# Optimization experiments

Hardware: AMD Instinct MI355X
Metric: run time of the kernel (lower is better)

## Reference

```python
import jax, jax.numpy as jnp
import numpy as np

B, C, H, W = 8, 512, 64, 64
DEPTH, HEADS = 4, 8


def setup_inputs() -> dict:
    key = jax.random.key(0)
    ks = jax.random.split(key, 7)
    s = 0.02
    return {
        "x": jax.random.normal(ks[0], (B, C, H, W), jnp.float32),
        # axial positional embeddings, emb dim at index 1: (1,C,H,1) and (1,C,1,W)
        "pos_h": jax.random.normal(ks[1], (C, H), jnp.float32) * s,
        "pos_w": jax.random.normal(ks[2], (C, W), jnp.float32) * s,
        # per layer, per axis (0=height, 1=width): q, kv, out projections
        "wq": jax.random.normal(ks[3], (DEPTH, 2, C, C), jnp.float32) * s,
        "wkv": jax.random.normal(ks[4], (DEPTH, 2, C, 2 * C), jnp.float32) * s,
        "wo": jax.random.normal(ks[5], (DEPTH, 2, C, C), jnp.float32) * s,
        "wo_b": jax.random.normal(ks[6], (DEPTH, 2, C), jnp.float32) * s,
    }


def _attn_last_axis(x, wq, wkv, wo, wo_b, heads):
    """Self-attention along the second-to-last axis. x: (..., L, C)."""
    lead = x.shape[:-2]
    L, Cd = x.shape[-2], x.shape[-1]
    e = Cd // heads
    q = x @ wq                       # (..., L, C)
    k, v = jnp.split(x @ wkv, 2, axis=-1)
    sh = lead + (L, heads, e)
    q, k, v = q.reshape(sh), k.reshape(sh), v.reshape(sh)
    dots = jnp.einsum('...ihe,...jhe->...hij', q, k) * (e ** -0.5)
    attn = jax.nn.softmax(dots, axis=-1)
    out = jnp.einsum('...hij,...jhe->...ihe', attn, v).reshape(lead + (L, heads * e))
    return out @ wo + wo_b


def reference(x, pos_h, pos_w, wq, wkv, wo, wo_b):
    # positional embedding: x + (1,C,H,1) + (1,C,1,W)
    x = x + pos_h[None, :, :, None] + pos_w[None, :, None, :]
    y = jnp.transpose(x, (0, 2, 3, 1))  # (B,H,W,C) channels-last working layout
    for l in range(DEPTH):
        # height-axis attention: (B,W,H,C), attend along H
        yh = jnp.transpose(y, (0, 2, 1, 3))
        oh = _attn_last_axis(yh, wq[l, 0], wkv[l, 0], wo[l, 0], wo_b[l, 0], HEADS)
        oh = jnp.transpose(oh, (0, 2, 1, 3))
        # width-axis attention: attend along W
        ow = _attn_last_axis(y, wq[l, 1], wkv[l, 1], wo[l, 1], wo_b[l, 1], HEADS)
        y = oh + ow  # sum_axial_out=True, no residual
    return jnp.transpose(y, (0, 3, 1, 2))  # back to (B,C,H,W)
```

## Files before the change

kernel.cpp:

```cpp
#include <hip/hip_runtime.h>
#include <stdint.h>


typedef __attribute__((ext_vector_type(8))) short bf16x8;
typedef __attribute__((ext_vector_type(4))) float f32x4;
typedef unsigned short u16;
typedef unsigned int u32;

#define MFMA16(a, b, c) __builtin_amdgcn_mfma_f32_16x16x32_bf16((a), (b), (c), 0, 0, 0)
#define SBAR() __builtin_amdgcn_sched_barrier(0)

__device__ __forceinline__ float b2f(u16 h) {
    u32 u = ((u32)h) << 16;
    float f;
    __builtin_memcpy(&f, &u, 4);
    return f;
}
__device__ __forceinline__ u16 f2b(float f) {
    u32 u;
    __builtin_memcpy(&u, &f, 4);
    u32 r = (u + 0x7fffu + ((u >> 16) & 1u)) >> 16;
    return (u16)r;
}
__device__ __forceinline__ uint2 pack4(const f32x4& v) {
    uint2 pk;
    pk.x = (u32)f2b(v[0]) | ((u32)f2b(v[1]) << 16);
    pk.y = (u32)f2b(v[2]) | ((u32)f2b(v[3]) << 16);
    return pk;
}

#define GLD_LDS16(g, l)                                                        \
    __builtin_amdgcn_global_load_lds(                                          \
        (const __attribute__((address_space(1))) void*)(g),                    \
        (__attribute__((address_space(3))) void*)(l), 16, 0, 0)

__global__ __launch_bounds__(256) void embed_kernel(
    const float* __restrict__ x, const float* __restrict__ ph,
    const float* __restrict__ pw, u16* __restrict__ y)
{
    __shared__ float tile[64][65];
    const int c0 = blockIdx.x * 64, h = blockIdx.y, b = blockIdx.z;
    const int t = threadIdx.x;
#pragma unroll
    for (int i = 0; i < 4; ++i) {
        int cl = (t >> 4) + i * 16;
        int w4 = (t & 15) * 4;
        const float* src = x + (((size_t)(b * 512 + c0 + cl)) * 64 + h) * 64 + w4;
        float4 v = *(const float4*)src;
        float p = ph[(c0 + cl) * 64 + h];
        tile[cl][w4 + 0] = v.x + p + pw[(c0 + cl) * 64 + w4 + 0];
        tile[cl][w4 + 1] = v.y + p + pw[(c0 + cl) * 64 + w4 + 1];
        tile[cl][w4 + 2] = v.z + p + pw[(c0 + cl) * 64 + w4 + 2];
        tile[cl][w4 + 3] = v.w + p + pw[(c0 + cl) * 64 + w4 + 3];
    }
    __syncthreads();
    const int wl = t >> 2, cb = (t & 3) * 16;
    bf16x8 o0, o1;
#pragma unroll
    for (int j = 0; j < 8; ++j) o0[j] = (short)f2b(tile[cb + j][wl]);
#pragma unroll
    for (int j = 0; j < 8; ++j) o1[j] = (short)f2b(tile[cb + 8 + j][wl]);
    u16* dst = y + (((size_t)(b * 64 + h) * 64 + wl) * 512 + c0 + cb);
    *(bf16x8*)dst = o0;
    *(bf16x8*)(dst + 8) = o1;
}

__global__ __launch_bounds__(256) void wtrans_kernel(
    const float* __restrict__ wq, const float* __restrict__ wkv,
    const float* __restrict__ wo, u16* __restrict__ wT)
{
    const int mid = blockIdx.z;
    const int l = mid / 6, rest = mid % 6, axis = rest / 3, which = rest % 3;
    const size_t la = (size_t)(l * 2 + axis);
    const float* src;
    int N;
    size_t doff;
    if (which == 0)      { src = wq  + la * 512 * 512;  N = 512;  doff = la * (2048 * 512); }
    else if (which == 1) { src = wkv + la * 512 * 1024; N = 1024; doff = la * (2048 * 512) + 512 * 512; }
    else                 { src = wo  + la * 512 * 512;  N = 512;  doff = la * (2048 * 512) + 512 * 512 + 1024 * 512; }
    const int n0 = blockIdx.y * 64;
    if (n0 >= N) return;
    const int k0 = blockIdx.x * 64;
    __shared__ float tile[64][65];
    const int t = threadIdx.x;
#pragma unroll
    for (int i = 0; i < 4; ++i) {
        int kl = (t >> 4) + i * 16;
        int n4 = (t & 15) * 4;
        float4 v = *(const float4*)(src + (size_t)(k0 + kl) * N + n0 + n4);
        tile[kl][n4 + 0] = v.x; tile[kl][n4 + 1] = v.y;
        tile[kl][n4 + 2] = v.z; tile[kl][n4 + 3] = v.w;
    }
    __syncthreads();
    const int nl = t >> 2, kb = (t & 3) * 16;
    bf16x8 o0, o1;
#pragma unroll
    for (int j = 0; j < 8; ++j) o0[j] = (short)f2b(tile[kb + j][nl]);
#pragma unroll
    for (int j = 0; j < 8; ++j) o1[j] = (short)f2b(tile[kb + 8 + j][nl]);
    u16* dst = wT + doff + (size_t)(n0 + nl) * 512 + k0 + kb;
    *(bf16x8*)dst = o0;
    *(bf16x8*)(dst + 8) = o1;
}

template <int AXIS>
__global__ __launch_bounds__(512, 2) void fused_layer(
    const u16* __restrict__ y,
    const u16* __restrict__ wTla,
    const float* __restrict__ bias,
    u16* __restrict__ yout)
{
    __shared__ u16 LDS[65536];
    const int tid = threadIdx.x, lane = tid & 63, wid = tid >> 6;
    const int l16 = lane & 15, g = lane >> 4;
    const int bid = blockIdx.x;
    const size_t rowbase = ((size_t)(bid >> 6) << 12) +
                           (AXIS == 0 ? (size_t)(bid & 63) : ((size_t)(bid & 63) << 6));
    const int rowstr = (AXIS == 0) ? 64 : 1;

    u16* Ys = LDS;
    u16* scr = LDS + 32768 + wid * 4096;

#pragma unroll
    for (int i = 0; i < 8; ++i) {
        int row = wid * 8 + i;
        const u16* src = y + (rowbase + (size_t)row * rowstr) * 512 + ((lane ^ (row & 7)) << 3);
        GLD_LDS16(src, Ys + row * 512);
    }
    __syncthreads();

    const int hoff = wid * 64;
    const u16* wq_ = wTla + (size_t)hoff * 512;
    const u16* wk_ = wTla + (size_t)(512 + hoff) * 512;
    const u16* wv_ = wTla + (size_t)(512 + 512 + hoff) * 512;
    const u16* wo_ = wTla + (size_t)(512 + 1024) * 512;

#define YF(r, t) (*(const bf16x8*)((const char*)Ys + (r) * 1024 + \
                    ((((t) * 4 + g) ^ ((r) & 7)) << 4)))
#define SF(r, k2) (*(const bf16x8*)((const char*)scr + (r) * 128 + \
                    (((k2) * 64 + g * 16) ^ (((r) & 7) << 4))))

    f32x4 ak[4][4] = {}, aq[4][4] = {};
#pragma unroll
    for (int t = 0; t < 16; ++t) {
        bf16x8 yf[4], wkf[4], wqf[4];
#pragma unroll
        for (int f = 0; f < 4; ++f) {
            int row = f * 16 + l16;
            yf[f]  = YF(row, t);
            wkf[f] = *(const bf16x8*)(wk_ + (size_t)row * 512 + t * 32 + g * 8);
            wqf[f] = *(const bf16x8*)(wq_ + (size_t)row * 512 + t * 32 + g * 8);
        }
#pragma unroll
        for (int ef = 0; ef < 4; ++ef)
#pragma unroll
            for (int jf = 0; jf < 4; ++jf) {
                ak[ef][jf] = MFMA16(wkf[ef], yf[jf], ak[ef][jf]);
                aq[ef][jf] = MFMA16(wqf[ef], yf[jf], aq[ef][jf]);
            }
    }

#pragma unroll
    for (int ef = 0; ef < 4; ++ef)
#pragma unroll
        for (int jf = 0; jf < 4; ++jf) {
            int j = jf * 16 + l16, bo = (ef * 16 + g * 4) * 2;
            *(uint2*)((char*)scr + j * 128 + (bo ^ ((j & 7) << 4))) = pack4(ak[ef][jf]);
        }
    SBAR();
    bf16x8 kf[4][2];
#pragma unroll
    for (int jf = 0; jf < 4; ++jf)
#pragma unroll
        for (int k2 = 0; k2 < 2; ++k2) kf[jf][k2] = SF(jf * 16 + l16, k2);
    SBAR();
#pragma unroll
    for (int ef = 0; ef < 4; ++ef)
#pragma unroll
        for (int jf = 0; jf < 4; ++jf) {
            int j = jf * 16 + l16, bo = (ef * 16 + g * 4) * 2;
            *(uint2*)((char*)scr + j * 128 + (bo ^ ((j & 7) << 4))) = pack4(aq[ef][jf]);
        }
    SBAR();
    bf16x8 qf[4][2];
#pragma unroll
    for (int if_ = 0; if_ < 4; ++if_)
#pragma unroll
        for (int k2 = 0; k2 < 2; ++k2) qf[if_][k2] = SF(if_ * 16 + l16, k2);
    SBAR();

    f32x4 st[4][4] = {};
#pragma unroll
    for (int k2 = 0; k2 < 2; ++k2)
#pragma unroll
        for (int i_f = 0; i_f < 4; ++i_f)
#pragma unroll
            for (int j_f = 0; j_f < 4; ++j_f)
                st[i_f][j_f] = MFMA16(kf[j_f][k2], qf[i_f][k2], st[i_f][j_f]);

#pragma unroll
    for (int i_f = 0; i_f < 4; ++i_f) {
        const int irow = i_f * 16 + l16;
        float ev[4][4];
        float mx = -1e30f;
#pragma unroll
        for (int j_f = 0; j_f < 4; ++j_f)
#pragma unroll
            for (int r = 0; r < 4; ++r) {
                float v = st[i_f][j_f][r] * 0.125f;
                ev[j_f][r] = v;
                mx = fmaxf(mx, v);
            }
        mx = fmaxf(mx, __shfl_xor(mx, 16, 64));
        mx = fmaxf(mx, __shfl_xor(mx, 32, 64));
        float sum = 0.f;
#pragma unroll
        for (int j_f = 0; j_f < 4; ++j_f)
#pragma unroll
            for (int r = 0; r < 4; ++r) {
                float e = __expf(ev[j_f][r] - mx);
                ev[j_f][r] = e;
                sum += e;
            }
        sum += __shfl_xor(sum, 16, 64);
        sum += __shfl_xor(sum, 32, 64);
        float inv = __builtin_amdgcn_rcpf(sum);
#pragma unroll
        for (int j_f = 0; j_f < 4; ++j_f) {
            uint2 pk;
            pk.x = (u32)f2b(ev[j_f][0] * inv) | ((u32)f2b(ev[j_f][1] * inv) << 16);
            pk.y = (u32)f2b(ev[j_f][2] * inv) | ((u32)f2b(ev[j_f][3] * inv) << 16);
            int addr = irow * 128 + ((j_f * 32 + g * 8) ^ ((irow & 7) << 4));
            *(uint2*)((char*)scr + addr) = pk;
        }
    }
    SBAR();
    bf16x8 pf[4][2];
#pragma unroll
    for (int if_ = 0; if_ < 4; ++if_)
#pragma unroll
        for (int k2 = 0; k2 < 2; ++k2) pf[if_][k2] = SF(if_ * 16 + l16, k2);
    SBAR();

    f32x4 av[4][4] = {};
#pragma unroll
    for (int t = 0; t < 16; ++t) {
        bf16x8 yf[4], wvf[4];
#pragma unroll
        for (int f = 0; f < 4; ++f) {
            int row = f * 16 + l16;
            yf[f]  = YF(row, t);
            wvf[f] = *(const bf16x8*)(wv_ + (size_t)row * 512 + t * 32 + g * 8);
        }
#pragma unroll
        for (int jf = 0; jf < 4; ++jf)
#pragma unroll
            for (int ef = 0; ef < 4; ++ef)
                av[jf][ef] = MFMA16(yf[jf], wvf[ef], av[jf][ef]);
    }
#pragma unroll
    for (int jf = 0; jf < 4; ++jf)
#pragma unroll
        for (int ef = 0; ef < 4; ++ef) {
            int e = ef * 16 + l16, bo = (jf * 16 + g * 4) * 2;
            *(uint2*)((char*)scr + e * 128 + (bo ^ ((e & 7) << 4))) = pack4(av[jf][ef]);
        }
    SBAR();
    bf16x8 vtf[4][2];
#pragma unroll
    for (int ef = 0; ef < 4; ++ef)
#pragma unroll
        for (int k2 = 0; k2 < 2; ++k2) vtf[ef][k2] = SF(ef * 16 + l16, k2);
    SBAR();

    f32x4 of[4][4] = {};
#pragma unroll
    for (int k2 = 0; k2 < 2; ++k2)
#pragma unroll
        for (int ef = 0; ef < 4; ++ef)
#pragma unroll
            for (int i_f = 0; i_f < 4; ++i_f)
                of[ef][i_f] = MFMA16(vtf[ef][k2], pf[i_f][k2], of[ef][i_f]);

    __syncthreads();
#pragma unroll
    for (int ef = 0; ef < 4; ++ef)
#pragma unroll
        for (int i_f = 0; i_f < 4; ++i_f) {
            int i = i_f * 16 + l16;
            int bo = (hoff + ef * 16 + g * 4) * 2;
            *(uint2*)((char*)Ys + i * 1024 + (bo ^ ((i & 7) << 4))) = pack4(of[ef][i_f]);
        }
    __syncthreads();

    const int n0 = hoff;
    f32x4 ao[4][4] = {};
#pragma unroll
    for (int t = 0; t < 16; ++t) {
        bf16x8 off[4], wof[4];
#pragma unroll
        for (int f = 0; f < 4; ++f) {
            int row = f * 16 + l16;
            off[f] = YF(row, t);
            wof[f] = *(const bf16x8*)(wo_ + (size_t)(n0 + row) * 512 + t * 32 + g * 8);
        }
#pragma unroll
        for (int nf = 0; nf < 4; ++nf)
#pragma unroll
            for (int if_ = 0; if_ < 4; ++if_)
                ao[nf][if_] = MFMA16(wof[nf], off[if_], ao[nf][if_]);
    }

    float4 b4[4];
#pragma unroll
    for (int nf = 0; nf < 4; ++nf) b4[nf] = *(const float4*)(bias + n0 + nf * 16 + g * 4);
#pragma unroll
    for (int if_ = 0; if_ < 4; ++if_) {
        const int i = if_ * 16 + l16;
        u16* dst = yout + (rowbase + (size_t)i * rowstr) * 512;
#pragma unroll
        for (int nf = 0; nf < 4; ++nf) {
            const int n = n0 + nf * 16 + g * 4;
            float v0 = ao[nf][if_][0] + b4[nf].x;
            float v1 = ao[nf][if_][1] + b4[nf].y;
            float v2 = ao[nf][if_][2] + b4[nf].z;
            float v3 = ao[nf][if_][3] + b4[nf].w;
            if (AXIS == 1) {
                ushort4 o = *(const ushort4*)(dst + n);
                v0 += b2f(o.x); v1 += b2f(o.y); v2 += b2f(o.z); v3 += b2f(o.w);
            }
            uint2 pk;
            pk.x = (u32)f2b(v0) | ((u32)f2b(v1) << 16);
            pk.y = (u32)f2b(v2) | ((u32)f2b(v3) << 16);
            *(uint2*)(dst + n) = pk;
        }
    }
#undef YF
#undef SF
}

__global__ __launch_bounds__(256) void untrans_kernel(
    const u16* __restrict__ y, float* __restrict__ out)
{
    __shared__ float tile[64][65];
    const int c0 = blockIdx.x * 64, h = blockIdx.y, b = blockIdx.z;
    const int t = threadIdx.x;
    {
        const int wl = t >> 2, cb = (t & 3) * 16;
        const u16* src = y + (((size_t)(b * 64 + h) * 64 + wl) * 512 + c0 + cb);
        bf16x8 v0 = *(const bf16x8*)src;
        bf16x8 v1 = *(const bf16x8*)(src + 8);
#pragma unroll
        for (int j = 0; j < 8; ++j) tile[wl][cb + j] = b2f((u16)v0[j]);
#pragma unroll
        for (int j = 0; j < 8; ++j) tile[wl][cb + 8 + j] = b2f((u16)v1[j]);
    }
    __syncthreads();
    const int cl = t >> 2, w16 = (t & 3) * 16;
    float* dst = out + (((size_t)(b * 512 + c0 + cl)) * 64 + h) * 64 + w16;
#pragma unroll
    for (int j = 0; j < 4; ++j) {
        float4 v;
        v.x = tile[w16 + j * 4 + 0][cl];
        v.y = tile[w16 + j * 4 + 1][cl];
        v.z = tile[w16 + j * 4 + 2][cl];
        v.w = tile[w16 + j * 4 + 3][cl];
        *(float4*)(dst + j * 4) = v;
    }
}

extern "C" void kernel_launch(void* const* d_in, const int* in_sizes, int n_in,
                              void* d_out, int out_size, void* d_ws, size_t ws_size,
                              hipStream_t stream)
{
    (void)in_sizes; (void)n_in; (void)out_size; (void)ws_size;
    const float* x   = (const float*)d_in[0];
    const float* ph  = (const float*)d_in[1];
    const float* pw  = (const float*)d_in[2];
    const float* wq  = (const float*)d_in[3];
    const float* wkv = (const float*)d_in[4];
    const float* wo  = (const float*)d_in[5];
    const float* wob = (const float*)d_in[6];

    char* ws = (char*)d_ws;
    u16* yA = (u16*)(ws);
    u16* yB = (u16*)(ws + 33554432);
    u16* wT = (u16*)(ws + 67108864);
    float* out = (float*)d_out;

    embed_kernel<<<dim3(8, 64, 8), 256, 0, stream>>>(x, ph, pw, yA);
    wtrans_kernel<<<dim3(8, 16, 24), 256, 0, stream>>>(wq, wkv, wo, wT);

    u16* yin = yA;
    u16* yout = yB;
    for (int l = 0; l < 4; ++l) {
        for (int axis = 0; axis < 2; ++axis) {
            const u16* wTla = wT + (size_t)(l * 2 + axis) * 2048 * 512;
            const float* bias = wob + (size_t)(l * 2 + axis) * 512;
            if (axis == 0)
                fused_layer<0><<<dim3(512), 512, 0, stream>>>(yin, wTla, bias, yout);
            else
                fused_layer<1><<<dim3(512), 512, 0, stream>>>(yin, wTla, bias, yout);
        }
        u16* tmp = yin; yin = yout; yout = tmp;
    }
    untrans_kernel<<<dim3(8, 64, 8), 256, 0, stream>>>(yin, out);
}
```

Before: 1.222 ms.

## Split K and Q projections and shrink per-wave scratch to cut LDS and registers

The fused axial-attention layer kernel now computes the K and Q projections in two separate passes that share one accumulator array, instead of one pass holding both. This halves live accumulator registers. Each wave's LDS scratch shrinks from 64 rows to 16 rows, and the transposes through scratch are done one 16-row fragment at a time. Total LDS per block drops from 128KB to 80KB. The goal is lower register and LDS pressure so more blocks or waves can be resident, at the cost of reading the Y tile from LDS twice for K and Q and having more small write/read rounds through scratch.

```diff
diff --git a/kernel.cpp b/kernel.cpp
--- a/kernel.cpp
+++ b/kernel.cpp
@@ -110,7 +110,7 @@
     const float* __restrict__ bias,
     u16* __restrict__ yout)
 {
-    __shared__ u16 LDS[65536];
+    __shared__ u16 LDS[40960];
     const int tid = threadIdx.x, lane = tid & 63, wid = tid >> 6;
     const int l16 = lane & 15, g = lane >> 4;
     const int bid = blockIdx.x;
@@ -119,7 +119,7 @@
     const int rowstr = (AXIS == 0) ? 64 : 1;
 
     u16* Ys = LDS;
-    u16* scr = LDS + 32768 + wid * 4096;
+    u16* scr = LDS + 32768 + wid * 1024;
 
 #pragma unroll
     for (int i = 0; i < 8; ++i) {
@@ -137,57 +137,72 @@
 
 #define YF(r, t) (*(const bf16x8*)((const char*)Ys + (r) * 1024 + \
                     ((((t) * 4 + g) ^ ((r) & 7)) << 4)))
-#define SF(r, k2) (*(const bf16x8*)((const char*)scr + (r) * 128 + \
-                    (((k2) * 64 + g * 16) ^ (((r) & 7) << 4))))
-
-    f32x4 ak[4][4] = {}, aq[4][4] = {};
+#define SW16(bo, val) *(uint2*)((char*)scr + l16 * 128 + ((bo) ^ ((l16 & 7) << 4))) = (val)
+#define SF16(k2) (*(const bf16x8*)((const char*)scr + l16 * 128 + \
+                    (((k2) * 64 + g * 16) ^ ((l16 & 7) << 4))))
+
+    f32x4 acc[4][4];
+    bf16x8 kf[4][2], qf[4][2];
+
+#pragma unroll
+    for (int ef = 0; ef < 4; ++ef)
+#pragma unroll
+        for (int jf = 0; jf < 4; ++jf) acc[ef][jf] = f32x4{0.f, 0.f, 0.f, 0.f};
 #pragma unroll
     for (int t = 0; t < 16; ++t) {
-        bf16x8 yf[4], wkf[4], wqf[4];
+        bf16x8 yf[4], wf[4];
 #pragma unroll
         for (int f = 0; f < 4; ++f) {
             int row = f * 16 + l16;
-            yf[f]  = YF(row, t);
-            wkf[f] = *(const bf16x8*)(wk_ + (size_t)row * 512 + t * 32 + g * 8);
-            wqf[f] = *(const bf16x8*)(wq_ + (size_t)row * 512 + t * 32 + g * 8);
+            yf[f] = YF(row, t);
+            wf[f] = *(const bf16x8*)(wk_ + (size_t)row * 512 + t * 32 + g * 8);
         }
 #pragma unroll
         for (int ef = 0; ef < 4; ++ef)
 #pragma unroll
-            for (int jf = 0; jf < 4; ++jf) {
-                ak[ef][jf] = MFMA16(wkf[ef], yf[jf], ak[ef][jf]);
-                aq[ef][jf] = MFMA16(wqf[ef], yf[jf], aq[ef][jf]);
-            }
+            for (int jf = 0; jf < 4; ++jf)
+                acc[ef][jf] = MFMA16(wf[ef], yf[jf], acc[ef][jf]);
+    }
+#pragma unroll
+    for (int jf = 0; jf < 4; ++jf) {
+#pragma unroll
+        for (int ef = 0; ef < 4; ++ef)
+            SW16((ef * 16 + g * 4) * 2, pack4(acc[ef][jf]));
+        SBAR();
+        kf[jf][0] = SF16(0);
+        kf[jf][1] = SF16(1);
+        SBAR();
     }
 
 #pragma unroll
     for (int ef = 0; ef < 4; ++ef)
 #pragma unroll
-        for (int jf = 0; jf < 4; ++jf) {
-            int j = jf * 16 + l16, bo = (ef * 16 + g * 4) * 2;
-            *(uint2*)((char*)scr + j * 128 + (bo ^ ((j & 7) << 4))) = pack4(ak[ef][jf]);
-        }
-    SBAR();
-    bf16x8 kf[4][2];
-#pragma unroll
-    for (int jf = 0; jf < 4; ++jf)
-#pragma unroll
-        for (int k2 = 0; k2 < 2; ++k2) kf[jf][k2] = SF(jf * 16 + l16, k2);
-    SBAR();
-#pragma unroll
-    for (int ef = 0; ef < 4; ++ef)
-#pragma unroll
-        for (int jf = 0; jf < 4; ++jf) {
-            int j = jf * 16 + l16, bo = (ef * 16 + g * 4) * 2;
-            *(uint2*)((char*)scr + j * 128 + (bo ^ ((j & 7) << 4))) = pack4(aq[ef][jf]);
-        }
-    SBAR();
-    bf16x8 qf[4][2];
-#pragma unroll
-    for (int if_ = 0; if_ < 4; ++if_)
-#pragma unroll
-        for (int k2 = 0; k2 < 2; ++k2) qf[if_][k2] = SF(if_ * 16 + l16, k2);
-    SBAR();
+        for (int jf = 0; jf < 4; ++jf) acc[ef][jf] = f32x4{0.f, 0.f, 0.f, 0.f};
+#pragma unroll
+    for (int t = 0; t < 16; ++t) {
+        bf16x8 yf[4], wf[4];
+#pragma unroll
+        for (int f = 0; f < 4; ++f) {
+            int row = f * 16 + l16;
+            yf[f] = YF(row, t);
+            wf[f] = *(const bf16x8*)(wq_ + (size_t)row * 512 + t * 32 + g * 8);
+        }
+#pragma unroll
+        for (int ef = 0; ef < 4; ++ef)
+#pragma unroll
+            for (int jf = 0; jf < 4; ++jf)
+                acc[ef][jf] = MFMA16(wf[ef], yf[jf], acc[ef][jf]);
+    }
+#pragma unroll
+    for (int jf = 0; jf < 4; ++jf) {
+#pragma unroll
+        for (int ef = 0; ef < 4; ++ef)
+            SW16((ef * 16 + g * 4) * 2, pack4(acc[ef][jf]));
+        SBAR();
+        qf[jf][0] = SF16(0);
+        qf[jf][1] = SF16(1);
+        SBAR();
+    }
 
     f32x4 st[4][4] = {};
 #pragma unroll
@@ -198,9 +213,9 @@
             for (int j_f = 0; j_f < 4; ++j_f)
                 st[i_f][j_f] = MFMA16(kf[j_f][k2], qf[i_f][k2], st[i_f][j_f]);
 
+    bf16x8 pf[4][2];
 #pragma unroll
     for (int i_f = 0; i_f < 4; ++i_f) {
-        const int irow = i_f * 16 + l16;
         float ev[4][4];
         float mx = -1e30f;
 #pragma unroll
@@ -230,48 +245,44 @@
             uint2 pk;
             pk.x = (u32)f2b(ev[j_f][0] * inv) | ((u32)f2b(ev[j_f][1] * inv) << 16);
             pk.y = (u32)f2b(ev[j_f][2] * inv) | ((u32)f2b(ev[j_f][3] * inv) << 16);
-            int addr = irow * 128 + ((j_f * 32 + g * 8) ^ ((irow & 7) << 4));
-            *(uint2*)((char*)scr + addr) = pk;
-        }
-    }
-    SBAR();
-    bf16x8 pf[4][2];
-#pragma unroll
-    for (int if_ = 0; if_ < 4; ++if_)
-#pragma unroll
-        for (int k2 = 0; k2 < 2; ++k2) pf[if_][k2] = SF(if_ * 16 + l16, k2);
-    SBAR();
-
-    f32x4 av[4][4] = {};
+            SW16(j_f * 32 + g * 8, pk);
+        }
+        SBAR();
+        pf[i_f][0] = SF16(0);
+        pf[i_f][1] = SF16(1);
+        SBAR();
+    }
+
+#pragma unroll
+    for (int jf = 0; jf < 4; ++jf)
+#pragma unroll
+        for (int ef = 0; ef < 4; ++ef) acc[jf][ef] = f32x4{0.f, 0.f, 0.f, 0.f};
 #pragma unroll
     for (int t = 0; t < 16; ++t) {
-        bf16x8 yf[4], wvf[4];
+        bf16x8 yf[4], wf[4];
 #pragma unroll
         for (int f = 0; f < 4; ++f) {
             int row = f * 16 + l16;
-            yf[f]  = YF(row, t);
-            wvf[f] = *(const bf16x8*)(wv_ + (size_t)row * 512 + t * 32 + g * 8);
+            yf[f] = YF(row, t);
+            wf[f] = *(const bf16x8*)(wv_ + (size_t)row * 512 + t * 32 + g * 8);
         }
 #pragma unroll
         for (int jf = 0; jf < 4; ++jf)
 #pragma unroll
             for (int ef = 0; ef < 4; ++ef)
-                av[jf][ef] = MFMA16(yf[jf], wvf[ef], av[jf][ef]);
-    }
-#pragma unroll
-    for (int jf = 0; jf < 4; ++jf)
-#pragma unroll
-        for (int ef = 0; ef < 4; ++ef) {
-            int e = ef * 16 + l16, bo = (jf * 16 + g * 4) * 2;
-            *(uint2*)((char*)scr + e * 128 + (bo ^ ((e & 7) << 4))) = pack4(av[jf][ef]);
-        }
-    SBAR();
+                acc[jf][ef] = MFMA16(yf[jf], wf[ef], acc[jf][ef]);
+    }
     bf16x8 vtf[4][2];
 #pragma unroll
-    for (int ef = 0; ef < 4; ++ef)
-#pragma unroll
-        for (int k2 = 0; k2 < 2; ++k2) vtf[ef][k2] = SF(ef * 16 + l16, k2);
-    SBAR();
+    for (int ef = 0; ef < 4; ++ef) {
+#pragma unroll
+        for (int jf = 0; jf < 4; ++jf)
+            SW16((jf * 16 + g * 4) * 2, pack4(acc[jf][ef]));
+        SBAR();
+        vtf[ef][0] = SF16(0);
+        vtf[ef][1] = SF16(1);
+        SBAR();
+    }
 
     f32x4 of[4][4] = {};
 #pragma unroll
@@ -293,38 +304,40 @@
         }
     __syncthreads();
 
-    const int n0 = hoff;
-    f32x4 ao[4][4] = {};
+#pragma unroll
+    for (int nf = 0; nf < 4; ++nf)
+#pragma unroll
+        for (int if_ = 0; if_ < 4; ++if_) acc[nf][if_] = f32x4{0.f, 0.f, 0.f, 0.f};
 #pragma unroll
     for (int t = 0; t < 16; ++t) {
-        bf16x8 off[4], wof[4];
+        bf16x8 off[4], wf[4];
 #pragma unroll
         for (int f = 0; f < 4; ++f) {
             int row = f * 16 + l16;
             off[f] = YF(row, t);
-            wof[f] = *(const bf16x8*)(wo_ + (size_t)(n0 + row) * 512 + t * 32 + g * 8);
+            wf[f] = *(const bf16x8*)(wo_ + (size_t)(hoff + row) * 512 + t * 32 + g * 8);
         }
 #pragma unroll
         for (int nf = 0; nf < 4; ++nf)
 #pragma unroll
             for (int if_ = 0; if_ < 4; ++if_)
-                ao[nf][if_] = MFMA16(wof[nf], off[if_], ao[nf][if_]);
+                acc[nf][if_] = MFMA16(wf[nf], off[if_], acc[nf][if_]);
     }
 
     float4 b4[4];
 #pragma unroll
-    for (int nf = 0; nf < 4; ++nf) b4[nf] = *(const float4*)(bias + n0 + nf * 16 + g * 4);
+    for (int nf = 0; nf < 4; ++nf) b4[nf] = *(const float4*)(bias + hoff + nf * 16 + g * 4);
 #pragma unroll
     for (int if_ = 0; if_ < 4; ++if_) {
         const int i = if_ * 16 + l16;
         u16* dst = yout + (rowbase + (size_t)i * rowstr) * 512;
 #pragma unroll
         for (int nf = 0; nf < 4; ++nf) {
-            const int n = n0 + nf * 16 + g * 4;
-            float v0 = ao[nf][if_][0] + b4[nf].x;
-            float v1 = ao[nf][if_][1] + b4[nf].y;
-            float v2 = ao[nf][if_][2] + b4[nf].z;
-            float v3 = ao[nf][if_][3] + b4[nf].w;
+            const int n = hoff + nf * 16 + g * 4;
+            float v0 = acc[nf][if_][0] + b4[nf].x;
+            float v1 = acc[nf][if_][1] + b4[nf].y;
+            float v2 = acc[nf][if_][2] + b4[nf].z;
+            float v3 = acc[nf][if_][3] + b4[nf].w;
             if (AXIS == 1) {
                 ushort4 o = *(const ushort4*)(dst + n);
                 v0 += b2f(o.x); v1 += b2f(o.y); v2 += b2f(o.z); v3 += b2f(o.w);
@@ -336,7 +349,8 @@
         }
     }
 #undef YF
-#undef SF
+#undef SW16
+#undef SF16
 }
 
 __global__ __launch_bounds__(256) void untrans_kernel(
```

After: 1.167 ms. -4.5%, faster.

## Split each attention head across two waves using 1024-thread blocks

Applied to the files above, without the earlier changes.

The fused axial attention kernel now runs 16 waves per block, with two waves per head. Each wave computes half of that head's K/Q/V projection columns and half of the query rows. K, Q and V tiles are shared through a per-head LDS region guarded by block-wide barriers, and the output projection is split into 32-column slices per wave. The aim is to cut per-wave register pressure and serial MFMA work so more waves can hide latency. The cost is extra __syncthreads, one block per CU under the launch bound, and each wave still reading all Y fragments for every projection.

```diff
diff --git a/kernel.cpp b/kernel.cpp
--- a/kernel.cpp
+++ b/kernel.cpp
@@ -104,7 +104,7 @@
 }
 
 template <int AXIS>
-__global__ __launch_bounds__(512, 2) void fused_layer(
+__global__ __launch_bounds__(1024, 1) void fused_layer(
     const u16* __restrict__ y,
     const u16* __restrict__ wTla,
     const float* __restrict__ bias,
@@ -113,213 +113,218 @@
     __shared__ u16 LDS[65536];
     const int tid = threadIdx.x, lane = tid & 63, wid = tid >> 6;
     const int l16 = lane & 15, g = lane >> 4;
+    const int head = wid >> 1, half = wid & 1, hbase = half * 32;
+    const int hoff = head * 64;
     const int bid = blockIdx.x;
     const size_t rowbase = ((size_t)(bid >> 6) << 12) +
                            (AXIS == 0 ? (size_t)(bid & 63) : ((size_t)(bid & 63) << 6));
     const int rowstr = (AXIS == 0) ? 64 : 1;
 
     u16* Ys = LDS;
-    u16* scr = LDS + 32768 + wid * 4096;
-
-#pragma unroll
-    for (int i = 0; i < 8; ++i) {
-        int row = wid * 8 + i;
+    u16* R  = LDS + 32768 + head * 4096;
+
+#pragma unroll
+    for (int i = 0; i < 4; ++i) {
+        int row = wid * 4 + i;
         const u16* src = y + (rowbase + (size_t)row * rowstr) * 512 + ((lane ^ (row & 7)) << 3);
         GLD_LDS16(src, Ys + row * 512);
     }
     __syncthreads();
 
-    const int hoff = wid * 64;
     const u16* wq_ = wTla + (size_t)hoff * 512;
     const u16* wk_ = wTla + (size_t)(512 + hoff) * 512;
-    const u16* wv_ = wTla + (size_t)(512 + 512 + hoff) * 512;
-    const u16* wo_ = wTla + (size_t)(512 + 1024) * 512;
+    const u16* wv_ = wTla + (size_t)(1024 + hoff) * 512;
+    const u16* wo_ = wTla + (size_t)(1536) * 512;
 
 #define YF(r, t) (*(const bf16x8*)((const char*)Ys + (r) * 1024 + \
                     ((((t) * 4 + g) ^ ((r) & 7)) << 4)))
-#define SF(r, k2) (*(const bf16x8*)((const char*)scr + (r) * 128 + \
-                    (((k2) * 64 + g * 16) ^ (((r) & 7) << 4))))
-
-    f32x4 ak[4][4] = {}, aq[4][4] = {};
+#define RW(row, bo, val) *(uint2*)((char*)R + (row) * 128 + \
+                    ((bo) ^ (((row) & 7) << 4))) = (val)
+#define RF(row, k2) (*(const bf16x8*)((const char*)R + (row) * 128 + \
+                    ((((k2) * 64 + g * 16)) ^ (((row) & 7) << 4))))
+
+    {
+        f32x4 ak[2][4] = {};
+#pragma unroll
+        for (int t = 0; t < 16; ++t) {
+            bf16x8 yf[4], wf[2];
+#pragma unroll
+            for (int f = 0; f < 4; ++f) yf[f] = YF(f * 16 + l16, t);
+#pragma unroll
+            for (int e = 0; e < 2; ++e)
+                wf[e] = *(const bf16x8*)(wk_ + (size_t)(hbase + e * 16 + l16) * 512 + t * 32 + g * 8);
+#pragma unroll
+            for (int e = 0; e < 2; ++e)
+#pragma unroll
+                for (int jf = 0; jf < 4; ++jf)
+                    ak[e][jf] = MFMA16(wf[e], yf[jf], ak[e][jf]);
+        }
+#pragma unroll
+        for (int e = 0; e < 2; ++e)
+#pragma unroll
+            for (int jf = 0; jf < 4; ++jf)
+                RW(jf * 16 + l16, hbase * 2 + e * 32 + g * 8, pack4(ak[e][jf]));
+    }
+    __syncthreads();
+
+    bf16x8 kf[4][2];
+#pragma unroll
+    for (int jf = 0; jf < 4; ++jf)
+#pragma unroll
+        for (int k2 = 0; k2 < 2; ++k2) kf[jf][k2] = RF(jf * 16 + l16, k2);
+
+    f32x4 aq[2][4] = {};
 #pragma unroll
     for (int t = 0; t < 16; ++t) {
-        bf16x8 yf[4], wkf[4], wqf[4];
-#pragma unroll
-        for (int f = 0; f < 4; ++f) {
-            int row = f * 16 + l16;
-            yf[f]  = YF(row, t);
-            wkf[f] = *(const bf16x8*)(wk_ + (size_t)row * 512 + t * 32 + g * 8);
-            wqf[f] = *(const bf16x8*)(wq_ + (size_t)row * 512 + t * 32 + g * 8);
-        }
-#pragma unroll
-        for (int ef = 0; ef < 4; ++ef)
-#pragma unroll
-            for (int jf = 0; jf < 4; ++jf) {
-                ak[ef][jf] = MFMA16(wkf[ef], yf[jf], ak[ef][jf]);
-                aq[ef][jf] = MFMA16(wqf[ef], yf[jf], aq[ef][jf]);
-            }
-    }
-
-#pragma unroll
-    for (int ef = 0; ef < 4; ++ef)
-#pragma unroll
-        for (int jf = 0; jf < 4; ++jf) {
-            int j = jf * 16 + l16, bo = (ef * 16 + g * 4) * 2;
-            *(uint2*)((char*)scr + j * 128 + (bo ^ ((j & 7) << 4))) = pack4(ak[ef][jf]);
-        }
-    SBAR();
-    bf16x8 kf[4][2];
-#pragma unroll
-    for (int jf = 0; jf < 4; ++jf)
-#pragma unroll
-        for (int k2 = 0; k2 < 2; ++k2) kf[jf][k2] = SF(jf * 16 + l16, k2);
-    SBAR();
-#pragma unroll
-    for (int ef = 0; ef < 4; ++ef)
-#pragma unroll
-        for (int jf = 0; jf < 4; ++jf) {
-            int j = jf * 16 + l16, bo = (ef * 16 + g * 4) * 2;
-            *(uint2*)((char*)scr + j * 128 + (bo ^ ((j & 7) << 4))) = pack4(aq[ef][jf]);
-        }
-    SBAR();
-    bf16x8 qf[4][2];
-#pragma unroll
-    for (int if_ = 0; if_ < 4; ++if_)
-#pragma unroll
-        for (int k2 = 0; k2 < 2; ++k2) qf[if_][k2] = SF(if_ * 16 + l16, k2);
-    SBAR();
-
-    f32x4 st[4][4] = {};
+        bf16x8 yf[4], wf[2];
+#pragma unroll
+        for (int f = 0; f < 4; ++f) yf[f] = YF(f * 16 + l16, t);
+#pragma unroll
+        for (int e = 0; e < 2; ++e)
+            wf[e] = *(const bf16x8*)(wq_ + (size_t)(hbase + e * 16 + l16) * 512 + t * 32 + g * 8);
+#pragma unroll
+        for (int e = 0; e < 2; ++e)
+#pragma unroll
+            for (int if_ = 0; if_ < 4; ++if_)
+                aq[e][if_] = MFMA16(wf[e], yf[if_], aq[e][if_]);
+    }
+    __syncthreads();
+#pragma unroll
+    for (int e = 0; e < 2; ++e)
+#pragma unroll
+        for (int if_ = 0; if_ < 4; ++if_)
+            RW(if_ * 16 + l16, hbase * 2 + e * 32 + g * 8, pack4(aq[e][if_]));
+    __syncthreads();
+
+    bf16x8 qf[2][2];
+#pragma unroll
+    for (int if_ = 0; if_ < 2; ++if_)
+#pragma unroll
+        for (int k2 = 0; k2 < 2; ++k2) qf[if_][k2] = RF(hbase + if_ * 16 + l16, k2);
+
+    f32x4 st[2][4] = {};
 #pragma unroll
     for (int k2 = 0; k2 < 2; ++k2)
 #pragma unroll
-        for (int i_f = 0; i_f < 4; ++i_f)
-#pragma unroll
-            for (int j_f = 0; j_f < 4; ++j_f)
-                st[i_f][j_f] = MFMA16(kf[j_f][k2], qf[i_f][k2], st[i_f][j_f]);
-
-#pragma unroll
-    for (int i_f = 0; i_f < 4; ++i_f) {
-        const int irow = i_f * 16 + l16;
+        for (int if_ = 0; if_ < 2; ++if_)
+#pragma unroll
+            for (int jf = 0; jf < 4; ++jf)
+                st[if_][jf] = MFMA16(kf[jf][k2], qf[if_][k2], st[if_][jf]);
+
+    bf16x8 pf[2][2];
+#pragma unroll
+    for (int if_ = 0; if_ < 2; ++if_) {
+        const int irow = hbase + if_ * 16 + l16;
         float ev[4][4];
         float mx = -1e30f;
 #pragma unroll
-        for (int j_f = 0; j_f < 4; ++j_f)
+        for (int jf = 0; jf < 4; ++jf)
 #pragma unroll
             for (int r = 0; r < 4; ++r) {
-                float v = st[i_f][j_f][r] * 0.125f;
-                ev[j_f][r] = v;
+                float v = st[if_][jf][r] * 0.125f;
+                ev[jf][r] = v;
                 mx = fmaxf(mx, v);
             }
         mx = fmaxf(mx, __shfl_xor(mx, 16, 64));
         mx = fmaxf(mx, __shfl_xor(mx, 32, 64));
         float sum = 0.f;
 #pragma unroll
-        for (int j_f = 0; j_f < 4; ++j_f)
+        for (int jf = 0; jf < 4; ++jf)
 #pragma unroll
             for (int r = 0; r < 4; ++r) {
-                float e = __expf(ev[j_f][r] - mx);
-                ev[j_f][r] = e;
+                float e = __expf(ev[jf][r] - mx);
+                ev[jf][r] = e;
                 sum += e;
             }
         sum += __shfl_xor(sum, 16, 64);
         sum += __shfl_xor(sum, 32, 64);
         float inv = __builtin_amdgcn_rcpf(sum);
 #pragma unroll
-        for (int j_f = 0; j_f < 4; ++j_f) {
+        for (int jf = 0; jf < 4; ++jf) {
             uint2 pk;
-            pk.x = (u32)f2b(ev[j_f][0] * inv) | ((u32)f2b(ev[j_f][1] * inv) << 16);
-            pk.y = (u32)f2b(ev[j_f][2] * inv) | ((u32)f2b(ev[j_f][3] * inv) << 16);
-            int addr = irow * 128 + ((j_f * 32 + g * 8) ^ ((irow & 7) << 4));
-            *(uint2*)((char*)scr + addr) = pk;
+            pk.x = (u32)f2b(ev[jf][0] * inv) | ((u32)f2b(ev[jf][1] * inv) << 16);
+            pk.y = (u32)f2b(ev[jf][2] * inv) | ((u32)f2b(ev[jf][3] * inv) << 16);
+            RW(irow, jf * 32 + g * 8, pk);
         }
-    }
-    SBAR();
-    bf16x8 pf[4][2];
-#pragma unroll
-    for (int if_ = 0; if_ < 4; ++if_)
-#pragma unroll
-        for (int k2 = 0; k2 < 2; ++k2) pf[if_][k2] = SF(if_ * 16 + l16, k2);
-    SBAR();
-
-    f32x4 av[4][4] = {};
+        SBAR();
+        pf[if_][0] = RF(irow, 0);
+        pf[if_][1] = RF(irow, 1);
+        SBAR();
+    }
+
+    f32x4 av[4][2] = {};
 #pragma unroll
     for (int t = 0; t < 16; ++t) {
-        bf16x8 yf[4], wvf[4];
-#pragma unroll
-        for (int f = 0; f < 4; ++f) {
-            int row = f * 16 + l16;
-            yf[f]  = YF(row, t);
-            wvf[f] = *(const bf16x8*)(wv_ + (size_t)row * 512 + t * 32 + g * 8);
+        bf16x8 yf[4], wf[2];
+#pragma unroll
+        for (int f = 0; f < 4; ++f) yf[f] = YF(f * 16 + l16, t);
+#pragma unroll
+        for (int e = 0; e < 2; ++e)
+            wf[e] = *(const bf16x8*)(wv_ + (size_t)(hbase + e * 16 + l16) * 512 + t * 32 + g * 8);
+#pragma unroll
+        for (int jf = 0; jf < 4; ++jf)
+#pragma unroll
+            for (int e = 0; e < 2; ++e)
+                av[jf][e] = MFMA16(yf[jf], wf[e], av[jf][e]);
+    }
+#pragma unroll
+    for (int e = 0; e < 2; ++e)
+#pragma unroll
+        for (int jf = 0; jf < 4; ++jf)
+            RW(hbase + e * 16 + l16, jf * 32 + g * 8, pack4(av[jf][e]));
+    __syncthreads();
+
+    bf16x8 vtf[4][2];
+#pragma unroll
+    for (int ef = 0; ef < 4; ++ef)
+#pragma unroll
+        for (int k2 = 0; k2 < 2; ++k2) vtf[ef][k2] = RF(ef * 16 + l16, k2);
+
+    f32x4 of[4][2] = {};
+#pragma unroll
+    for (int k2 = 0; k2 < 2; ++k2)
+#pragma unroll
+        for (int ef = 0; ef < 4; ++ef)
+#pragma unroll
+            for (int if_ = 0; if_ < 2; ++if_)
+                of[ef][if_] = MFMA16(vtf[ef][k2], pf[if_][k2], of[ef][if_]);
+
+#pragma unroll
+    for (int ef = 0; ef < 4; ++ef)
+#pragma unroll
+        for (int if_ = 0; if_ < 2; ++if_) {
+            int i = hbase + if_ * 16 + l16;
+            int bo = (hoff + ef * 16 + g * 4) * 2;
+            *(uint2*)((char*)Ys + i * 1024 + (bo ^ ((i & 7) << 4))) = pack4(of[ef][if_]);
         }
-#pragma unroll
-        for (int jf = 0; jf < 4; ++jf)
-#pragma unroll
-            for (int ef = 0; ef < 4; ++ef)
-                av[jf][ef] = MFMA16(yf[jf], wvf[ef], av[jf][ef]);
-    }
-#pragma unroll
-    for (int jf = 0; jf < 4; ++jf)
-#pragma unroll
-        for (int ef = 0; ef < 4; ++ef) {
-            int e = ef * 16 + l16, bo = (jf * 16 + g * 4) * 2;
-            *(uint2*)((char*)scr + e * 128 + (bo ^ ((e & 7) << 4))) = pack4(av[jf][ef]);
-        }
-    SBAR();
-    bf16x8 vtf[4][2];
-#pragma unroll
-    for (int ef = 0; ef < 4; ++ef)
-#pragma unroll
-        for (int k2 = 0; k2 < 2; ++k2) vtf[ef][k2] = SF(ef * 16 + l16, k2);
-    SBAR();
-
-    f32x4 of[4][4] = {};
-#pragma unroll
-    for (int k2 = 0; k2 < 2; ++k2)
-#pragma unroll
-        for (int ef = 0; ef < 4; ++ef)
-#pragma unroll
-            for (int i_f = 0; i_f < 4; ++i_f)
-                of[ef][i_f] = MFMA16(vtf[ef][k2], pf[i_f][k2], of[ef][i_f]);
-
-    __syncthreads();
-#pragma unroll
-    for (int ef = 0; ef < 4; ++ef)
-#pragma unroll
-        for (int i_f = 0; i_f < 4; ++i_f) {
-            int i = i_f * 16 + l16;
-            int bo = (hoff + ef * 16 + g * 4) * 2;
-            *(uint2*)((char*)Ys + i * 1024 + (bo ^ ((i & 7) << 4))) = pack4(of[ef][i_f]);
-        }
-    __syncthreads();
-
-    const int n0 = hoff;
-    f32x4 ao[4][4] = {};
+    __syncthreads();
+
+    const int n0 = wid * 32;
+    f32x4 ao[2][4] = {};
 #pragma unroll
     for (int t = 0; t < 16; ++t) {
-        bf16x8 off[4], wof[4];
-#pragma unroll
-        for (int f = 0; f < 4; ++f) {
-            int row = f * 16 + l16;
-            off[f] = YF(row, t);
-            wof[f] = *(const bf16x8*)(wo_ + (size_t)(n0 + row) * 512 + t * 32 + g * 8);
-        }
-#pragma unroll
-        for (int nf = 0; nf < 4; ++nf)
+        bf16x8 off[4], wf[2];
+#pragma unroll
+        for (int f = 0; f < 4; ++f) off[f] = YF(f * 16 + l16, t);
+#pragma unroll
+        for (int nf = 0; nf < 2; ++nf)
+            wf[nf] = *(const bf16x8*)(wo_ + (size_t)(n0 + nf * 16 + l16) * 512 + t * 32 + g * 8);
+#pragma unroll
+        for (int nf = 0; nf < 2; ++nf)
 #pragma unroll
             for (int if_ = 0; if_ < 4; ++if_)
-                ao[nf][if_] = MFMA16(wof[nf], off[if_], ao[nf][if_]);
-    }
-
-    float4 b4[4];
-#pragma unroll
-    for (int nf = 0; nf < 4; ++nf) b4[nf] = *(const float4*)(bias + n0 + nf * 16 + g * 4);
+                ao[nf][if_] = MFMA16(wf[nf], off[if_], ao[nf][if_]);
+    }
+
+    float4 b4[2];
+#pragma unroll
+    for (int nf = 0; nf < 2; ++nf) b4[nf] = *(const float4*)(bias + n0 + nf * 16 + g * 4);
 #pragma unroll
     for (int if_ = 0; if_ < 4; ++if_) {
         const int i = if_ * 16 + l16;
         u16* dst = yout + (rowbase + (size_t)i * rowstr) * 512;
 #pragma unroll
-        for (int nf = 0; nf < 4; ++nf) {
+        for (int nf = 0; nf < 2; ++nf) {
             const int n = n0 + nf * 16 + g * 4;
             float v0 = ao[nf][if_][0] + b4[nf].x;
             float v1 = ao[nf][if_][1] + b4[nf].y;
@@ -336,7 +341,8 @@
         }
     }
 #undef YF
-#undef SF
+#undef RW
+#undef RF
 }
 
 __global__ __launch_bounds__(256) void untrans_kernel(
@@ -398,9 +404,9 @@
             const u16* wTla = wT + (size_t)(l * 2 + axis) * 2048 * 512;
             const float* bias = wob + (size_t)(l * 2 + axis) * 512;
             if (axis == 0)
-                fused_layer<0><<<dim3(512), 512, 0, stream>>>(yin, wTla, bias, yout);
+                fused_layer<0><<<dim3(512), 1024, 0, stream>>>(yin, wTla, bias, yout);
             else
-                fused_layer<1><<<dim3(512), 512, 0, stream>>>(yin, wTla, bias, yout);
+                fused_layer<1><<<dim3(512), 1024, 0, stream>>>(yin, wTla, bias, yout);
         }
         u16* tmp = yin; yin = yout; yout = tmp;
     }
```

After: 1.192 ms. 2.4% less time.
